# Performance work log

Hardware: AMD Instinct MI355X
Metric: run time of the kernel (lower is better)

## Reference

```python
import jax, jax.numpy as jnp
import numpy as np


def setup_inputs() -> dict:
    key = jax.random.key(0)
    k1, k2, k3, k4 = jax.random.split(key, 4)
    M, K, N = 64, 8192, 28672
    group_size = 128
    num_groups = K // group_size  # 64
    x = jax.random.normal(k1, (M, K), dtype=jnp.float16)
    # packed int4: each int32 holds one byte value in [0, 256) = two 4-bit nibbles
    weight_packed = jax.random.randint(k2, (N, K // 2), 0, 256, dtype=jnp.int32)
    # small positive per-group scales, typical of int4 quantization
    scales = (jax.random.uniform(k3, (N, num_groups), dtype=jnp.float16) * jnp.float16(0.02)
              + jnp.float16(0.001))
    bias = jax.random.normal(k4, (N,), dtype=jnp.float16) * jnp.float16(0.1)
    return {"x": x, "weight_packed": weight_packed, "scales": scales,
            "bias": bias, "group_size": group_size}


def reference(x, weight_packed, scales, bias, group_size):
    # x: [M, K] fp16; weight_packed: [N, K//2] bytes; scales: [N, K//group_size] fp16
    N, Khalf = weight_packed.shape
    K = 2 * Khalf
    num_groups = K // group_size
    # unpack nibbles: low nibble = even K index, high nibble = odd K index
    low = weight_packed & 0xF
    high = (weight_packed >> 4) & 0xF
    w_int = jnp.stack([low, high], axis=-1).reshape(N, K)  # [N, K] in [0, 16)
    # dequantize with zero-point 8 and per-group scales
    w = (w_int.astype(jnp.float16) - jnp.float16(8.0)).reshape(N, num_groups, group_size)
    w = (w * scales[:, :, None]).reshape(N, K)  # [N, K] fp16
    out = jnp.einsum("mk,nk->mn", x, w)  # [M, N] fp16
    return out + bias[None, :]
```

## Files before the change

### kernel.cpp

```cpp
#include <hip/hip_runtime.h>
#include <stdint.h>


typedef __attribute__((ext_vector_type(8))) short     short8;
typedef __attribute__((ext_vector_type(4))) float     f32x4;
typedef __attribute__((ext_vector_type(4))) int       i32x4;
typedef __attribute__((ext_vector_type(2))) _Float16  f16x2;
typedef __attribute__((ext_vector_type(8))) _Float16  f16x8;

static __device__ __forceinline__ void gload_lds16(const void* gp, void* lp) {
    __builtin_amdgcn_global_load_lds(
        (const __attribute__((address_space(1))) unsigned int*)gp,
        (__attribute__((address_space(3))) unsigned int*)lp, 16, 0, 0);
}

static __device__ __forceinline__ f16x8 dequant(const i32x4& w, f16x2 s2) {
    const f16x2 c1032 = {(_Float16)1032.0f, (_Float16)1032.0f};
    union { unsigned u[4]; f16x8 v; } r;
    #pragma unroll
    for (int j = 0; j < 4; ++j) {
        unsigned v = (unsigned)w[j];
        unsigned u = ((v & 0xFu) | 0x64006400u) | ((v << 12) & 0xF0000u);
        f16x2 h = __builtin_bit_cast(f16x2, u);
        h = (h - c1032) * s2;
        r.u[j] = __builtin_bit_cast(unsigned, h);
    }
    return r.v;
}

__global__ __launch_bounds__(256)
void xpack_kernel(const float* __restrict__ x, unsigned short* __restrict__ xf, int K) {
    int c    = blockIdx.x * 256 + threadIdx.x;
    int g    = c >> 10;
    int st   = (c >> 8) & 3;
    int mt   = (c >> 6) & 3;
    int lane = c & 63;
    int quad = lane >> 4, l15 = lane & 15;
    const float* p = x + (size_t)(l15 + mt * 16) * K + g * 128 + st * 32 + quad * 8;
    f32x4 lo = *(const f32x4*)p;
    f32x4 hi = *(const f32x4*)(p + 4);
    f16x8 r = { (_Float16)lo[0], (_Float16)lo[1], (_Float16)lo[2], (_Float16)lo[3],
                (_Float16)hi[0], (_Float16)hi[1], (_Float16)hi[2], (_Float16)hi[3] };
    *(short8*)(xf + (size_t)c * 8) = __builtin_bit_cast(short8, r);
}

__global__ __launch_bounds__(256)
void int4mm_kernel(const unsigned short* __restrict__ xf,
                   const int*   __restrict__ wp,
                   const float* __restrict__ sc,
                   const float* __restrict__ bias,
                   float*       __restrict__ out,
                   int K, int N)
{
    __shared__ char lds[49152];
    char*  ldsW = lds;
    float* ldsS = (float*)(lds + 32768);

    const int tid  = threadIdx.x;
    const int lane = tid & 63;
    const int wave = tid >> 6;
    const int quad = lane >> 4;
    const int l15  = lane & 15;
    const int blk64 = blockIdx.x * 64;
    const int ng   = K / 128;

    const char* wp8 = (const char*)wp;

    unsigned woff[4];
    #pragma unroll
    for (int j = 0; j < 4; ++j) {
        int cloc  = wave * 16 + j * 4 + quad;
        int chunk = l15 ^ (j * 4 + quad);
        woff[j] = ((unsigned)(blk64 + cloc) << 14) + ((unsigned)chunk << 4);
    }

    int rdW[4];
    #pragma unroll
    for (int nt = 0; nt < 4; ++nt)
        rdW[nt] = (nt * 16 + l15) * 256 + (((wave * 4 + quad) ^ l15) << 4);

    {
        const int c  = tid & 63;
        const int g0 = (tid >> 6) * 16;
        const float* sp = sc + (size_t)(blk64 + c) * ng + g0;
        f32x4 s0 = *(const f32x4*)(sp);
        f32x4 s1 = *(const f32x4*)(sp + 4);
        f32x4 s2 = *(const f32x4*)(sp + 8);
        f32x4 s3 = *(const f32x4*)(sp + 12);
        #pragma unroll
        for (int j = 0; j < 4; ++j) {
            ldsS[(g0 + 0  + j) * 64 + c] = s0[j];
            ldsS[(g0 + 4  + j) * 64 + c] = s1[j];
            ldsS[(g0 + 8  + j) * 64 + c] = s2[j];
            ldsS[(g0 + 12 + j) * 64 + c] = s3[j];
        }
    }
    #pragma unroll
    for (int j = 0; j < 4; ++j)
        gload_lds16(wp8 + woff[j], ldsW + (wave * 4 + j) * 1024);

    const char* xbase = (const char*)xf + wave * 4096 + lane * 16;
    f16x8 xn[4], xc[4];
    #pragma unroll
    for (int mt = 0; mt < 4; ++mt)
        xn[mt] = *(const f16x8*)(xbase + mt * 1024);

    f32x4 acc[4][4];
    #pragma unroll
    for (int mt = 0; mt < 4; ++mt)
        #pragma unroll
        for (int nt = 0; nt < 4; ++nt)
            acc[mt][nt] = f32x4{0.f, 0.f, 0.f, 0.f};

    __syncthreads();

    #pragma unroll 1
    for (int g = 0; g < ng; ++g) {
        const int p  = g & 1;
        const int gn = (g + 1 < ng) ? g + 1 : ng - 1;

        #pragma unroll
        for (int mt = 0; mt < 4; ++mt) xc[mt] = xn[mt];

        const char* xs = xbase + (size_t)gn * 16384;
        #pragma unroll
        for (int mt = 0; mt < 4; ++mt)
            xn[mt] = *(const f16x8*)(xs + mt * 1024);

        __builtin_amdgcn_s_barrier();

        #pragma unroll
        for (int j = 0; j < 4; ++j)
            gload_lds16(wp8 + woff[j] + (size_t)gn * 256,
                        ldsW + (p ^ 1) * 16384 + (wave * 4 + j) * 1024);

        asm volatile("s_waitcnt vmcnt(8)" ::: "memory");
        __builtin_amdgcn_s_barrier();
        __builtin_amdgcn_sched_barrier(0);

        const char* wb = ldsW + p * 16384;
        i32x4 v0 = *(const i32x4*)(wb + rdW[0]);
        i32x4 v1 = *(const i32x4*)(wb + rdW[1]);
        i32x4 v2 = *(const i32x4*)(wb + rdW[2]);
        i32x4 v3 = *(const i32x4*)(wb + rdW[3]);

        const float* sg = ldsS + g * 64;
        const float sf0 = sg[l15], sf1 = sg[16 + l15];
        const float sf2 = sg[32 + l15], sf3 = sg[48 + l15];

        {
            f16x8 b = dequant(v0, f16x2{(_Float16)sf0, (_Float16)sf0});
            #pragma unroll
            for (int mt = 0; mt < 4; ++mt)
                acc[mt][0] = __builtin_amdgcn_mfma_f32_16x16x32_f16(xc[mt], b, acc[mt][0], 0, 0, 0);
        }
        {
            f16x8 b = dequant(v1, f16x2{(_Float16)sf1, (_Float16)sf1});
            #pragma unroll
            for (int mt = 0; mt < 4; ++mt)
                acc[mt][1] = __builtin_amdgcn_mfma_f32_16x16x32_f16(xc[mt], b, acc[mt][1], 0, 0, 0);
        }
        {
            f16x8 b = dequant(v2, f16x2{(_Float16)sf2, (_Float16)sf2});
            #pragma unroll
            for (int mt = 0; mt < 4; ++mt)
                acc[mt][2] = __builtin_amdgcn_mfma_f32_16x16x32_f16(xc[mt], b, acc[mt][2], 0, 0, 0);
        }
        {
            f16x8 b = dequant(v3, f16x2{(_Float16)sf3, (_Float16)sf3});
            #pragma unroll
            for (int mt = 0; mt < 4; ++mt)
                acc[mt][3] = __builtin_amdgcn_mfma_f32_16x16x32_f16(xc[mt], b, acc[mt][3], 0, 0, 0);
        }
    }

    __syncthreads();
    #pragma unroll
    for (int o = 0; o < 4; ++o) {
        if (o == wave) continue;
        const int s = wave - (wave > o ? 1 : 0);
        #pragma unroll
        for (int nt = 0; nt < 4; ++nt)
            *(f32x4*)(lds + (size_t)(((o * 3 + s) * 4 + nt) * 1024) + lane * 16)
                = acc[o][nt];
    }
    __syncthreads();

    f32x4 own[4];
    #pragma unroll
    for (int nt = 0; nt < 4; ++nt) own[nt] = acc[0][nt];
    #pragma unroll
    for (int o = 1; o < 4; ++o)
        if (wave == o) {
            own[0] = acc[o][0]; own[1] = acc[o][1];
            own[2] = acc[o][2]; own[3] = acc[o][3];
        }
    #pragma unroll
    for (int s = 0; s < 3; ++s)
        #pragma unroll
        for (int nt = 0; nt < 4; ++nt)
            own[nt] += *(const f32x4*)(lds + (size_t)(((wave * 3 + s) * 4 + nt) * 1024)
                                       + lane * 16);

    #pragma unroll
    for (int nt = 0; nt < 4; ++nt) {
        const int col = blk64 + nt * 16 + l15;
        const float bv = bias[col];
        #pragma unroll
        for (int r = 0; r < 4; ++r)
            out[(size_t)(wave * 16 + quad * 4 + r) * N + col] = own[nt][r] + bv;
    }
}

extern "C" void kernel_launch(void* const* d_in, const int* in_sizes, int n_in,
                              void* d_out, int out_size, void* d_ws, size_t ws_size,
                              hipStream_t stream)
{
    const float* x    = (const float*)d_in[0];
    const int*   wp   = (const int*)d_in[1];
    const float* sc   = (const float*)d_in[2];
    const float* bias = (const float*)d_in[3];
    float*       out  = (float*)d_out;

    const int N  = in_sizes[3];
    const long long Kh = (long long)in_sizes[1] / N;
    const int K  = (int)(2 * Kh);
    const int ng = K / 128;

    unsigned short* xf = (unsigned short*)d_ws;

    xpack_kernel<<<(ng * 1024) / 256, 256, 0, stream>>>(x, xf, K);
    int4mm_kernel<<<N / 64, 256, 0, stream>>>(xf, wp, sc, bias, out, K, N);
}
```

Measured before the change: 107.2 us.

## Shrink int4 GEMM block tile from 64 to 16 output columns for more blocks

Each block now computes 16 output columns instead of 64. That gives four times as many blocks (1792 instead of 448), cuts LDS use from 48KB to 12KB, and adds a launch-bounds hint for 4 blocks per SM so occupancy rises. The goal is better latency hiding and fuller use of the 256 CUs in this memory-bound weight stream. The cost is that every block re-reads all of x, which is four times more activation traffic (served from L2), and there are fewer MFMAs per barrier per iteration.

```diff
diff --git a/kernel.cpp b/kernel.cpp
--- a/kernel.cpp
+++ b/kernel.cpp
@@ -44,7 +44,7 @@
     *(short8*)(xf + (size_t)c * 8) = __builtin_bit_cast(short8, r);
 }
 
-__global__ __launch_bounds__(256)
+__global__ __launch_bounds__(256, 4)
 void int4mm_kernel(const unsigned short* __restrict__ xf,
                    const int*   __restrict__ wp,
                    const float* __restrict__ sc,
@@ -52,52 +52,37 @@
                    float*       __restrict__ out,
                    int K, int N)
 {
-    __shared__ char lds[49152];
+    __shared__ char lds[12288];
     char*  ldsW = lds;
-    float* ldsS = (float*)(lds + 32768);
+    float* ldsS = (float*)(lds + 8192);
 
     const int tid  = threadIdx.x;
     const int lane = tid & 63;
     const int wave = tid >> 6;
     const int quad = lane >> 4;
     const int l15  = lane & 15;
-    const int blk64 = blockIdx.x * 64;
+    const int blk16 = blockIdx.x * 16;
     const int ng   = K / 128;
 
     const char* wp8 = (const char*)wp;
 
-    unsigned woff[4];
-    #pragma unroll
-    for (int j = 0; j < 4; ++j) {
-        int cloc  = wave * 16 + j * 4 + quad;
-        int chunk = l15 ^ (j * 4 + quad);
-        woff[j] = ((unsigned)(blk64 + cloc) << 14) + ((unsigned)chunk << 4);
-    }
+    const int cloc = wave * 4 + (lane >> 4);
+    const size_t wsrc = (size_t)(blk16 + cloc) * 16384
+                      + ((size_t)(unsigned)(l15 ^ cloc) << 4);
 
-    int rdW[4];
-    #pragma unroll
-    for (int nt = 0; nt < 4; ++nt)
-        rdW[nt] = (nt * 16 + l15) * 256 + (((wave * 4 + quad) ^ l15) << 4);
+    const int q   = wave * 4 + quad;
+    const int rdW = l15 * 256 + ((q ^ l15) << 4);
 
     {
-        const int c  = tid & 63;
-        const int g0 = (tid >> 6) * 16;
-        const float* sp = sc + (size_t)(blk64 + c) * ng + g0;
-        f32x4 s0 = *(const f32x4*)(sp);
-        f32x4 s1 = *(const f32x4*)(sp + 4);
-        f32x4 s2 = *(const f32x4*)(sp + 8);
-        f32x4 s3 = *(const f32x4*)(sp + 12);
+        const int c  = tid & 15;
+        const int g0 = (tid >> 4) * 4;
+        const float* sp = sc + (size_t)(blk16 + c) * ng + g0;
+        f32x4 s = *(const f32x4*)sp;
         #pragma unroll
-        for (int j = 0; j < 4; ++j) {
-            ldsS[(g0 + 0  + j) * 64 + c] = s0[j];
-            ldsS[(g0 + 4  + j) * 64 + c] = s1[j];
-            ldsS[(g0 + 8  + j) * 64 + c] = s2[j];
-            ldsS[(g0 + 12 + j) * 64 + c] = s3[j];
-        }
+        for (int j = 0; j < 4; ++j)
+            ldsS[(g0 + j) * 16 + c] = s[j];
     }
-    #pragma unroll
-    for (int j = 0; j < 4; ++j)
-        gload_lds16(wp8 + woff[j], ldsW + (wave * 4 + j) * 1024);
+    gload_lds16(wp8 + wsrc, ldsW + wave * 1024);
 
     const char* xbase = (const char*)xf + wave * 4096 + lane * 16;
     f16x8 xn[4], xc[4];
@@ -105,12 +90,10 @@
     for (int mt = 0; mt < 4; ++mt)
         xn[mt] = *(const f16x8*)(xbase + mt * 1024);
 
-    f32x4 acc[4][4];
+    f32x4 acc[4];
     #pragma unroll
     for (int mt = 0; mt < 4; ++mt)
-        #pragma unroll
-        for (int nt = 0; nt < 4; ++nt)
-            acc[mt][nt] = f32x4{0.f, 0.f, 0.f, 0.f};
+        acc[mt] = f32x4{0.f, 0.f, 0.f, 0.f};
 
     __syncthreads();
 
@@ -129,49 +112,19 @@
 
         __builtin_amdgcn_s_barrier();
 
-        #pragma unroll
-        for (int j = 0; j < 4; ++j)
-            gload_lds16(wp8 + woff[j] + (size_t)gn * 256,
-                        ldsW + (p ^ 1) * 16384 + (wave * 4 + j) * 1024);
+        gload_lds16(wp8 + wsrc + (size_t)gn * 256,
+                    ldsW + (p ^ 1) * 4096 + wave * 1024);
 
-        asm volatile("s_waitcnt vmcnt(8)" ::: "memory");
+        asm volatile("s_waitcnt vmcnt(5)" ::: "memory");
         __builtin_amdgcn_s_barrier();
         __builtin_amdgcn_sched_barrier(0);
 
-        const char* wb = ldsW + p * 16384;
-        i32x4 v0 = *(const i32x4*)(wb + rdW[0]);
-        i32x4 v1 = *(const i32x4*)(wb + rdW[1]);
-        i32x4 v2 = *(const i32x4*)(wb + rdW[2]);
-        i32x4 v3 = *(const i32x4*)(wb + rdW[3]);
-
-        const float* sg = ldsS + g * 64;
-        const float sf0 = sg[l15], sf1 = sg[16 + l15];
-        const float sf2 = sg[32 + l15], sf3 = sg[48 + l15];
-
-        {
-            f16x8 b = dequant(v0, f16x2{(_Float16)sf0, (_Float16)sf0});
-            #pragma unroll
-            for (int mt = 0; mt < 4; ++mt)
-                acc[mt][0] = __builtin_amdgcn_mfma_f32_16x16x32_f16(xc[mt], b, acc[mt][0], 0, 0, 0);
-        }
-        {
-            f16x8 b = dequant(v1, f16x2{(_Float16)sf1, (_Float16)sf1});
-            #pragma unroll
-            for (int mt = 0; mt < 4; ++mt)
-                acc[mt][1] = __builtin_amdgcn_mfma_f32_16x16x32_f16(xc[mt], b, acc[mt][1], 0, 0, 0);
-        }
-        {
-            f16x8 b = dequant(v2, f16x2{(_Float16)sf2, (_Float16)sf2});
-            #pragma unroll
-            for (int mt = 0; mt < 4; ++mt)
-                acc[mt][2] = __builtin_amdgcn_mfma_f32_16x16x32_f16(xc[mt], b, acc[mt][2], 0, 0, 0);
-        }
-        {
-            f16x8 b = dequant(v3, f16x2{(_Float16)sf3, (_Float16)sf3});
-            #pragma unroll
-            for (int mt = 0; mt < 4; ++mt)
-                acc[mt][3] = __builtin_amdgcn_mfma_f32_16x16x32_f16(xc[mt], b, acc[mt][3], 0, 0, 0);
-        }
+        i32x4 v = *(const i32x4*)(ldsW + p * 4096 + rdW);
+        const float sf = ldsS[g * 16 + l15];
+        f16x8 b = dequant(v, f16x2{(_Float16)sf, (_Float16)sf});
+        #pragma unroll
+        for (int mt = 0; mt < 4; ++mt)
+            acc[mt] = __builtin_amdgcn_mfma_f32_16x16x32_f16(xc[mt], b, acc[mt], 0, 0, 0);
     }
 
     __syncthreads();
@@ -179,37 +132,23 @@
     for (int o = 0; o < 4; ++o) {
         if (o == wave) continue;
         const int s = wave - (wave > o ? 1 : 0);
-        #pragma unroll
-        for (int nt = 0; nt < 4; ++nt)
-            *(f32x4*)(lds + (size_t)(((o * 3 + s) * 4 + nt) * 1024) + lane * 16)
-                = acc[o][nt];
+        *(f32x4*)(lds + (size_t)((o * 3 + s) * 1024) + lane * 16) = acc[o];
     }
     __syncthreads();
 
-    f32x4 own[4];
-    #pragma unroll
-    for (int nt = 0; nt < 4; ++nt) own[nt] = acc[0][nt];
+    f32x4 own = acc[0];
     #pragma unroll
     for (int o = 1; o < 4; ++o)
-        if (wave == o) {
-            own[0] = acc[o][0]; own[1] = acc[o][1];
-            own[2] = acc[o][2]; own[3] = acc[o][3];
-        }
+        if (wave == o) own = acc[o];
     #pragma unroll
     for (int s = 0; s < 3; ++s)
-        #pragma unroll
-        for (int nt = 0; nt < 4; ++nt)
-            own[nt] += *(const f32x4*)(lds + (size_t)(((wave * 3 + s) * 4 + nt) * 1024)
-                                       + lane * 16);
+        own += *(const f32x4*)(lds + (size_t)((wave * 3 + s) * 1024) + lane * 16);
 
+    const int col = blk16 + l15;
+    const float bv = bias[col];
     #pragma unroll
-    for (int nt = 0; nt < 4; ++nt) {
-        const int col = blk64 + nt * 16 + l15;
-        const float bv = bias[col];
-        #pragma unroll
-        for (int r = 0; r < 4; ++r)
-            out[(size_t)(wave * 16 + quad * 4 + r) * N + col] = own[nt][r] + bv;
-    }
+    for (int r = 0; r < 4; ++r)
+        out[(size_t)(wave * 16 + quad * 4 + r) * N + col] = own[r] + bv;
 }
 
 extern "C" void kernel_launch(void* const* d_in, const int* in_sizes, int n_in,
@@ -230,5 +169,5 @@
     unsigned short* xf = (unsigned short*)d_ws;
 
     xpack_kernel<<<(ng * 1024) / 256, 256, 0, stream>>>(x, xf, K);
-    int4mm_kernel<<<N / 64, 256, 0, stream>>>(xf, wp, sc, bias, out, K, N);
+    int4mm_kernel<<<N / 16, 256, 0, stream>>>(xf, wp, sc, bias, out, K, N);
 }
```

After: 162.3 us. 1.51x slower.

## Process two K-groups per pipeline stage with larger double-buffered weight tiles

Applied to the files above, without the earlier changes.

The main loop now covers two 128-wide K groups per iteration, staging 32KB of packed weights per buffer (64KB double-buffered). This halves the number of barrier pairs and makes each async load batch larger, so more bytes are in flight per wave. The four dequants per group are done up front before the MFMA block, and the x fragments for the next stage are loaded after use. LDS grows to 80KB and launch bounds request 2 blocks per CU, which may limit occupancy and add register pressure.

```diff
diff --git a/kernel.cpp b/kernel.cpp
--- a/kernel.cpp
+++ b/kernel.cpp
@@ -44,7 +44,7 @@
     *(short8*)(xf + (size_t)c * 8) = __builtin_bit_cast(short8, r);
 }
 
-__global__ __launch_bounds__(256)
+__global__ __launch_bounds__(256, 2)
 void int4mm_kernel(const unsigned short* __restrict__ xf,
                    const int*   __restrict__ wp,
                    const float* __restrict__ sc,
@@ -52,9 +52,9 @@
                    float*       __restrict__ out,
                    int K, int N)
 {
-    __shared__ char lds[49152];
+    __shared__ char lds[81920];
     char*  ldsW = lds;
-    float* ldsS = (float*)(lds + 32768);
+    float* ldsS = (float*)(lds + 65536);
 
     const int tid  = threadIdx.x;
     const int lane = tid & 63;
@@ -63,21 +63,26 @@
     const int l15  = lane & 15;
     const int blk64 = blockIdx.x * 64;
     const int ng   = K / 128;
+    const int ns   = ng / 2;
 
     const char* wp8 = (const char*)wp;
 
-    unsigned woff[4];
-    #pragma unroll
-    for (int j = 0; j < 4; ++j) {
-        int cloc  = wave * 16 + j * 4 + quad;
-        int chunk = l15 ^ (j * 4 + quad);
+    unsigned woff[8];
+    #pragma unroll
+    for (int j = 0; j < 8; ++j) {
+        const int cloc  = (wave * 8 + j) * 2 + (lane >> 5);
+        const int chunk = (lane & 31) ^ (cloc & 31);
         woff[j] = ((unsigned)(blk64 + cloc) << 14) + ((unsigned)chunk << 4);
     }
 
-    int rdW[4];
-    #pragma unroll
-    for (int nt = 0; nt < 4; ++nt)
-        rdW[nt] = (nt * 16 + l15) * 256 + (((wave * 4 + quad) ^ l15) << 4);
+    const int q = wave * 4 + quad;
+    int rdA[4], rdB[4];
+    #pragma unroll
+    for (int nt = 0; nt < 4; ++nt) {
+        const int base = (nt * 16 + l15) * 512 + ((q ^ l15) << 4);
+        rdA[nt] = base + (((0 ^ (nt & 1)) * 16) << 4);
+        rdB[nt] = base + (((1 ^ (nt & 1)) * 16) << 4);
+    }
 
     {
         const int c  = tid & 63;
@@ -96,14 +101,17 @@
         }
     }
     #pragma unroll
-    for (int j = 0; j < 4; ++j)
-        gload_lds16(wp8 + woff[j], ldsW + (wave * 4 + j) * 1024);
+    for (int j = 0; j < 8; ++j)
+        gload_lds16(wp8 + woff[j], ldsW + (wave * 8 + j) * 1024);
 
     const char* xbase = (const char*)xf + wave * 4096 + lane * 16;
-    f16x8 xn[4], xc[4];
+    f16x8 xa[4], xb[4];
     #pragma unroll
     for (int mt = 0; mt < 4; ++mt)
-        xn[mt] = *(const f16x8*)(xbase + mt * 1024);
+        xa[mt] = *(const f16x8*)(xbase + mt * 1024);
+    #pragma unroll
+    for (int mt = 0; mt < 4; ++mt)
+        xb[mt] = *(const f16x8*)(xbase + 16384 + mt * 1024);
 
     f32x4 acc[4][4];
     #pragma unroll
@@ -115,62 +123,73 @@
     __syncthreads();
 
     #pragma unroll 1
-    for (int g = 0; g < ng; ++g) {
-        const int p  = g & 1;
-        const int gn = (g + 1 < ng) ? g + 1 : ng - 1;
-
-        #pragma unroll
-        for (int mt = 0; mt < 4; ++mt) xc[mt] = xn[mt];
-
-        const char* xs = xbase + (size_t)gn * 16384;
-        #pragma unroll
-        for (int mt = 0; mt < 4; ++mt)
-            xn[mt] = *(const f16x8*)(xs + mt * 1024);
+    for (int s = 0; s < ns; ++s) {
+        const int p  = s & 1;
+        const int sn = (s + 1 < ns) ? s + 1 : ns - 1;
+        const int gA = 2 * s, gB = 2 * s + 1;
+        const int nA = (gA + 2 < ng) ? gA + 2 : ng - 1;
+        const int nB = (gB + 2 < ng) ? gB + 2 : ng - 1;
 
         __builtin_amdgcn_s_barrier();
 
         #pragma unroll
-        for (int j = 0; j < 4; ++j)
-            gload_lds16(wp8 + woff[j] + (size_t)gn * 256,
-                        ldsW + (p ^ 1) * 16384 + (wave * 4 + j) * 1024);
-
-        asm volatile("s_waitcnt vmcnt(8)" ::: "memory");
+        for (int j = 0; j < 8; ++j)
+            gload_lds16(wp8 + woff[j] + (size_t)sn * 512,
+                        ldsW + (p ^ 1) * 32768 + (wave * 8 + j) * 1024);
+
+        asm volatile("s_waitcnt vmcnt(16)" ::: "memory");
         __builtin_amdgcn_s_barrier();
         __builtin_amdgcn_sched_barrier(0);
 
-        const char* wb = ldsW + p * 16384;
-        i32x4 v0 = *(const i32x4*)(wb + rdW[0]);
-        i32x4 v1 = *(const i32x4*)(wb + rdW[1]);
-        i32x4 v2 = *(const i32x4*)(wb + rdW[2]);
-        i32x4 v3 = *(const i32x4*)(wb + rdW[3]);
-
-        const float* sg = ldsS + g * 64;
-        const float sf0 = sg[l15], sf1 = sg[16 + l15];
-        const float sf2 = sg[32 + l15], sf3 = sg[48 + l15];
+        const char* wb = ldsW + p * 32768;
+        const float* sgA = ldsS + gA * 64;
+        const float* sgB = ldsS + gB * 64;
 
         {
-            f16x8 b = dequant(v0, f16x2{(_Float16)sf0, (_Float16)sf0});
+            i32x4 v0 = *(const i32x4*)(wb + rdA[0]);
+            i32x4 v1 = *(const i32x4*)(wb + rdA[1]);
+            i32x4 v2 = *(const i32x4*)(wb + rdA[2]);
+            i32x4 v3 = *(const i32x4*)(wb + rdA[3]);
+            const float sf0 = sgA[l15], sf1 = sgA[16 + l15];
+            const float sf2 = sgA[32 + l15], sf3 = sgA[48 + l15];
+            f16x8 b0 = dequant(v0, f16x2{(_Float16)sf0, (_Float16)sf0});
+            f16x8 b1 = dequant(v1, f16x2{(_Float16)sf1, (_Float16)sf1});
+            f16x8 b2 = dequant(v2, f16x2{(_Float16)sf2, (_Float16)sf2});
+            f16x8 b3 = dequant(v3, f16x2{(_Float16)sf3, (_Float16)sf3});
+            #pragma unroll
+            for (int mt = 0; mt < 4; ++mt) {
+                acc[mt][0] = __builtin_amdgcn_mfma_f32_16x16x32_f16(xa[mt], b0, acc[mt][0], 0, 0, 0);
+                acc[mt][1] = __builtin_amdgcn_mfma_f32_16x16x32_f16(xa[mt], b1, acc[mt][1], 0, 0, 0);
+                acc[mt][2] = __builtin_amdgcn_mfma_f32_16x16x32_f16(xa[mt], b2, acc[mt][2], 0, 0, 0);
+                acc[mt][3] = __builtin_amdgcn_mfma_f32_16x16x32_f16(xa[mt], b3, acc[mt][3], 0, 0, 0);
+            }
+            const char* xs = xbase + (size_t)nA * 16384;
             #pragma unroll
             for (int mt = 0; mt < 4; ++mt)
-                acc[mt][0] = __builtin_amdgcn_mfma_f32_16x16x32_f16(xc[mt], b, acc[mt][0], 0, 0, 0);
+                xa[mt] = *(const f16x8*)(xs + mt * 1024);
         }
         {
-            f16x8 b = dequant(v1, f16x2{(_Float16)sf1, (_Float16)sf1});
+            i32x4 v0 = *(const i32x4*)(wb + rdB[0]);
+            i32x4 v1 = *(const i32x4*)(wb + rdB[1]);
+            i32x4 v2 = *(const i32x4*)(wb + rdB[2]);
+            i32x4 v3 = *(const i32x4*)(wb + rdB[3]);
+            const float sf0 = sgB[l15], sf1 = sgB[16 + l15];
+            const float sf2 = sgB[32 + l15], sf3 = sgB[48 + l15];
+            f16x8 b0 = dequant(v0, f16x2{(_Float16)sf0, (_Float16)sf0});
+            f16x8 b1 = dequant(v1, f16x2{(_Float16)sf1, (_Float16)sf1});
+            f16x8 b2 = dequant(v2, f16x2{(_Float16)sf2, (_Float16)sf2});
+            f16x8 b3 = dequant(v3, f16x2{(_Float16)sf3, (_Float16)sf3});
+            #pragma unroll
+            for (int mt = 0; mt < 4; ++mt) {
+                acc[mt][0] = __builtin_amdgcn_mfma_f32_16x16x32_f16(xb[mt], b0, acc[mt][0], 0, 0, 0);
+                acc[mt][1] = __builtin_amdgcn_mfma_f32_16x16x32_f16(xb[mt], b1, acc[mt][1], 0, 0, 0);
+                acc[mt][2] = __builtin_amdgcn_mfma_f32_16x16x32_f16(xb[mt], b2, acc[mt][2], 0, 0, 0);
+                acc[mt][3] = __builtin_amdgcn_mfma_f32_16x16x32_f16(xb[mt], b3, acc[mt][3], 0, 0, 0);
+            }
+            const char* xs = xbase + (size_t)nB * 16384;
             #pragma unroll
             for (int mt = 0; mt < 4; ++mt)
-                acc[mt][1] = __builtin_amdgcn_mfma_f32_16x16x32_f16(xc[mt], b, acc[mt][1], 0, 0, 0);
-        }
-        {
-            f16x8 b = dequant(v2, f16x2{(_Float16)sf2, (_Float16)sf2});
-            #pragma unroll
-            for (int mt = 0; mt < 4; ++mt)
-                acc[mt][2] = __builtin_amdgcn_mfma_f32_16x16x32_f16(xc[mt], b, acc[mt][2], 0, 0, 0);
-        }
-        {
-            f16x8 b = dequant(v3, f16x2{(_Float16)sf3, (_Float16)sf3});
-            #pragma unroll
-            for (int mt = 0; mt < 4; ++mt)
-                acc[mt][3] = __builtin_amdgcn_mfma_f32_16x16x32_f16(xc[mt], b, acc[mt][3], 0, 0, 0);
+                xb[mt] = *(const f16x8*)(xs + mt * 1024);
         }
     }
 
```

New measurement: 104.5 us. 1.03x faster.

## Split int4 GEMM into producer/consumer waves with LDS ring and atomic flags

Applied to the files above, without the earlier changes.

The main kernel now runs 8 waves: 4 producer waves stream packed weights into a 4-slot LDS ring with global_load_lds, and 4 consumer waves dequantize and issue MFMAs. Block-wide barriers are replaced by workgroup-scope atomic counters. Scales are pre-transposed by a new kernel so consumers can load them directly from global memory with prefetch. This aims to hide weight-load latency behind compute, at the cost of spin-wait overhead, an extra kernel launch, and more LDS per block, which may reduce occupancy.

```diff
diff --git a/kernel.cpp b/kernel.cpp
--- a/kernel.cpp
+++ b/kernel.cpp
@@ -7,6 +7,8 @@
 typedef __attribute__((ext_vector_type(4))) int       i32x4;
 typedef __attribute__((ext_vector_type(2))) _Float16  f16x2;
 typedef __attribute__((ext_vector_type(8))) _Float16  f16x8;
+
+#define RING 4
 
 static __device__ __forceinline__ void gload_lds16(const void* gp, void* lp) {
     __builtin_amdgcn_global_load_lds(
@@ -26,6 +28,11 @@
         r.u[j] = __builtin_bit_cast(unsigned, h);
     }
     return r.v;
+}
+
+static __device__ __forceinline__ void signal1(int* f, int lane) {
+    if (lane == 0)
+        __hip_atomic_fetch_add(f, 1, __ATOMIC_RELEASE, __HIP_MEMORY_SCOPE_WORKGROUP);
 }
 
 __global__ __launch_bounds__(256)
@@ -45,65 +52,33 @@
 }
 
 __global__ __launch_bounds__(256)
+void strans_kernel(const float* __restrict__ sc, float* __restrict__ sct, int N, int ng) {
+    int n = blockIdx.x * 256 + threadIdx.x;
+    int g = blockIdx.y;
+    sct[(size_t)g * N + n] = sc[(size_t)n * ng + g];
+}
+
+__global__ __launch_bounds__(512, 4)
 void int4mm_kernel(const unsigned short* __restrict__ xf,
                    const int*   __restrict__ wp,
-                   const float* __restrict__ sc,
+                   const float* __restrict__ sct,
                    const float* __restrict__ bias,
                    float*       __restrict__ out,
                    int K, int N)
 {
-    __shared__ char lds[49152];
-    char*  ldsW = lds;
-    float* ldsS = (float*)(lds + 32768);
+    __shared__ char ldsW[RING * 16384];
+    __shared__ int  prodDone[64];
+    __shared__ int  consDone[64];
 
     const int tid  = threadIdx.x;
+    const int wave = tid >> 6;
     const int lane = tid & 63;
-    const int wave = tid >> 6;
     const int quad = lane >> 4;
     const int l15  = lane & 15;
     const int blk64 = blockIdx.x * 64;
     const int ng   = K / 128;
 
-    const char* wp8 = (const char*)wp;
-
-    unsigned woff[4];
-    #pragma unroll
-    for (int j = 0; j < 4; ++j) {
-        int cloc  = wave * 16 + j * 4 + quad;
-        int chunk = l15 ^ (j * 4 + quad);
-        woff[j] = ((unsigned)(blk64 + cloc) << 14) + ((unsigned)chunk << 4);
-    }
-
-    int rdW[4];
-    #pragma unroll
-    for (int nt = 0; nt < 4; ++nt)
-        rdW[nt] = (nt * 16 + l15) * 256 + (((wave * 4 + quad) ^ l15) << 4);
-
-    {
-        const int c  = tid & 63;
-        const int g0 = (tid >> 6) * 16;
-        const float* sp = sc + (size_t)(blk64 + c) * ng + g0;
-        f32x4 s0 = *(const f32x4*)(sp);
-        f32x4 s1 = *(const f32x4*)(sp + 4);
-        f32x4 s2 = *(const f32x4*)(sp + 8);
-        f32x4 s3 = *(const f32x4*)(sp + 12);
-        #pragma unroll
-        for (int j = 0; j < 4; ++j) {
-            ldsS[(g0 + 0  + j) * 64 + c] = s0[j];
-            ldsS[(g0 + 4  + j) * 64 + c] = s1[j];
-            ldsS[(g0 + 8  + j) * 64 + c] = s2[j];
-            ldsS[(g0 + 12 + j) * 64 + c] = s3[j];
-        }
-    }
-    #pragma unroll
-    for (int j = 0; j < 4; ++j)
-        gload_lds16(wp8 + woff[j], ldsW + (wave * 4 + j) * 1024);
-
-    const char* xbase = (const char*)xf + wave * 4096 + lane * 16;
-    f16x8 xn[4], xc[4];
-    #pragma unroll
-    for (int mt = 0; mt < 4; ++mt)
-        xn[mt] = *(const f16x8*)(xbase + mt * 1024);
+    if (tid < 64) { prodDone[tid] = 0; consDone[tid] = 0; }
 
     f32x4 acc[4][4];
     #pragma unroll
@@ -114,101 +89,150 @@
 
     __syncthreads();
 
-    #pragma unroll 1
-    for (int g = 0; g < ng; ++g) {
-        const int p  = g & 1;
-        const int gn = (g + 1 < ng) ? g + 1 : ng - 1;
-
-        #pragma unroll
-        for (int mt = 0; mt < 4; ++mt) xc[mt] = xn[mt];
-
-        const char* xs = xbase + (size_t)gn * 16384;
+    if (wave < 4) {
+        const int p = wave;
+        const char* wp8 = (const char*)wp;
+        unsigned woff[4];
+        #pragma unroll
+        for (int j = 0; j < 4; ++j) {
+            const int cloc  = p * 16 + j * 4 + quad;
+            const int chunk = l15 ^ (j * 4 + quad);
+            woff[j] = ((unsigned)(blk64 + cloc) << 14) + ((unsigned)chunk << 4);
+        }
+        #pragma unroll 1
+        for (int g = 0; g < ng; ++g) {
+            if (g >= RING) {
+                while (__hip_atomic_load(&consDone[g - RING], __ATOMIC_ACQUIRE,
+                                         __HIP_MEMORY_SCOPE_WORKGROUP) < 4)
+                    __builtin_amdgcn_s_sleep(1);
+            }
+            char* slot = ldsW + (size_t)(g & (RING - 1)) * 16384;
+            #pragma unroll
+            for (int j = 0; j < 4; ++j)
+                gload_lds16(wp8 + woff[j] + (size_t)g * 256,
+                            slot + (p * 4 + j) * 1024);
+            asm volatile("s_waitcnt vmcnt(8)" ::: "memory");
+            if (g >= 2) signal1(&prodDone[g - 2], lane);
+        }
+        asm volatile("s_waitcnt vmcnt(4)" ::: "memory");
+        signal1(&prodDone[ng - 2], lane);
+        asm volatile("s_waitcnt vmcnt(0)" ::: "memory");
+        signal1(&prodDone[ng - 1], lane);
+    } else {
+        const int kst = wave - 4;
+        const int q   = kst * 4 + quad;
+        int rdW[4];
+        #pragma unroll
+        for (int nt = 0; nt < 4; ++nt)
+            rdW[nt] = (nt * 16 + l15) * 256 + ((q ^ l15) << 4);
+
+        const char* xbase = (const char*)xf + kst * 4096 + lane * 16;
+        f16x8 xn[4];
         #pragma unroll
         for (int mt = 0; mt < 4; ++mt)
-            xn[mt] = *(const f16x8*)(xs + mt * 1024);
-
-        __builtin_amdgcn_s_barrier();
-
-        #pragma unroll
-        for (int j = 0; j < 4; ++j)
-            gload_lds16(wp8 + woff[j] + (size_t)gn * 256,
-                        ldsW + (p ^ 1) * 16384 + (wave * 4 + j) * 1024);
-
-        asm volatile("s_waitcnt vmcnt(8)" ::: "memory");
-        __builtin_amdgcn_s_barrier();
-        __builtin_amdgcn_sched_barrier(0);
-
-        const char* wb = ldsW + p * 16384;
-        i32x4 v0 = *(const i32x4*)(wb + rdW[0]);
-        i32x4 v1 = *(const i32x4*)(wb + rdW[1]);
-        i32x4 v2 = *(const i32x4*)(wb + rdW[2]);
-        i32x4 v3 = *(const i32x4*)(wb + rdW[3]);
-
-        const float* sg = ldsS + g * 64;
-        const float sf0 = sg[l15], sf1 = sg[16 + l15];
-        const float sf2 = sg[32 + l15], sf3 = sg[48 + l15];
-
-        {
-            f16x8 b = dequant(v0, f16x2{(_Float16)sf0, (_Float16)sf0});
+            xn[mt] = *(const f16x8*)(xbase + mt * 1024);
+
+        float sfn[4], sfu[4];
+        #pragma unroll
+        for (int nt = 0; nt < 4; ++nt)
+            sfn[nt] = sct[blk64 + nt * 16 + l15];
+
+        #pragma unroll 1
+        for (int g = 0; g < ng; ++g) {
+            const int gn = (g + 1 < ng) ? g + 1 : ng - 1;
+
+            while (__hip_atomic_load(&prodDone[g], __ATOMIC_ACQUIRE,
+                                     __HIP_MEMORY_SCOPE_WORKGROUP) < 4)
+                __builtin_amdgcn_s_sleep(1);
+            __builtin_amdgcn_sched_barrier(0);
+
+            const char* wb = ldsW + (size_t)(g & (RING - 1)) * 16384;
+            i32x4 v0 = *(const i32x4*)(wb + rdW[0]);
+            i32x4 v1 = *(const i32x4*)(wb + rdW[1]);
+            i32x4 v2 = *(const i32x4*)(wb + rdW[2]);
+            i32x4 v3 = *(const i32x4*)(wb + rdW[3]);
+
+            #pragma unroll
+            for (int nt = 0; nt < 4; ++nt) sfu[nt] = sfn[nt];
+            const float* sp = sct + (size_t)gn * N + blk64;
+            #pragma unroll
+            for (int nt = 0; nt < 4; ++nt)
+                sfn[nt] = sp[nt * 16 + l15];
+
+            {
+                f16x8 b = dequant(v0, f16x2{(_Float16)sfu[0], (_Float16)sfu[0]});
+                #pragma unroll
+                for (int mt = 0; mt < 4; ++mt)
+                    acc[mt][0] = __builtin_amdgcn_mfma_f32_16x16x32_f16(xn[mt], b, acc[mt][0], 0, 0, 0);
+            }
+            {
+                f16x8 b = dequant(v1, f16x2{(_Float16)sfu[1], (_Float16)sfu[1]});
+                #pragma unroll
+                for (int mt = 0; mt < 4; ++mt)
+                    acc[mt][1] = __builtin_amdgcn_mfma_f32_16x16x32_f16(xn[mt], b, acc[mt][1], 0, 0, 0);
+            }
+            {
+                f16x8 b = dequant(v2, f16x2{(_Float16)sfu[2], (_Float16)sfu[2]});
+                #pragma unroll
+                for (int mt = 0; mt < 4; ++mt)
+                    acc[mt][2] = __builtin_amdgcn_mfma_f32_16x16x32_f16(xn[mt], b, acc[mt][2], 0, 0, 0);
+            }
+            {
+                f16x8 b = dequant(v3, f16x2{(_Float16)sfu[3], (_Float16)sfu[3]});
+                #pragma unroll
+                for (int mt = 0; mt < 4; ++mt)
+                    acc[mt][3] = __builtin_amdgcn_mfma_f32_16x16x32_f16(xn[mt], b, acc[mt][3], 0, 0, 0);
+            }
+
+            asm volatile("s_waitcnt lgkmcnt(0)" ::: "memory");
+            signal1(&consDone[g], lane);
+
+            const char* xs = xbase + (size_t)gn * 16384;
             #pragma unroll
             for (int mt = 0; mt < 4; ++mt)
-                acc[mt][0] = __builtin_amdgcn_mfma_f32_16x16x32_f16(xc[mt], b, acc[mt][0], 0, 0, 0);
-        }
-        {
-            f16x8 b = dequant(v1, f16x2{(_Float16)sf1, (_Float16)sf1});
-            #pragma unroll
-            for (int mt = 0; mt < 4; ++mt)
-                acc[mt][1] = __builtin_amdgcn_mfma_f32_16x16x32_f16(xc[mt], b, acc[mt][1], 0, 0, 0);
-        }
-        {
-            f16x8 b = dequant(v2, f16x2{(_Float16)sf2, (_Float16)sf2});
-            #pragma unroll
-            for (int mt = 0; mt < 4; ++mt)
-                acc[mt][2] = __builtin_amdgcn_mfma_f32_16x16x32_f16(xc[mt], b, acc[mt][2], 0, 0, 0);
-        }
-        {
-            f16x8 b = dequant(v3, f16x2{(_Float16)sf3, (_Float16)sf3});
-            #pragma unroll
-            for (int mt = 0; mt < 4; ++mt)
-                acc[mt][3] = __builtin_amdgcn_mfma_f32_16x16x32_f16(xc[mt], b, acc[mt][3], 0, 0, 0);
+                xn[mt] = *(const f16x8*)(xs + mt * 1024);
         }
     }
 
     __syncthreads();
-    #pragma unroll
-    for (int o = 0; o < 4; ++o) {
-        if (o == wave) continue;
-        const int s = wave - (wave > o ? 1 : 0);
-        #pragma unroll
-        for (int nt = 0; nt < 4; ++nt)
-            *(f32x4*)(lds + (size_t)(((o * 3 + s) * 4 + nt) * 1024) + lane * 16)
-                = acc[o][nt];
+    if (wave >= 4) {
+        const int kst = wave - 4;
+        #pragma unroll
+        for (int o = 0; o < 4; ++o) {
+            if (o == kst) continue;
+            const int s = kst - (kst > o ? 1 : 0);
+            #pragma unroll
+            for (int nt = 0; nt < 4; ++nt)
+                *(f32x4*)(ldsW + (size_t)(((o * 3 + s) * 4 + nt) * 1024) + lane * 16)
+                    = acc[o][nt];
+        }
     }
     __syncthreads();
-
-    f32x4 own[4];
-    #pragma unroll
-    for (int nt = 0; nt < 4; ++nt) own[nt] = acc[0][nt];
-    #pragma unroll
-    for (int o = 1; o < 4; ++o)
-        if (wave == o) {
-            own[0] = acc[o][0]; own[1] = acc[o][1];
-            own[2] = acc[o][2]; own[3] = acc[o][3];
-        }
-    #pragma unroll
-    for (int s = 0; s < 3; ++s)
-        #pragma unroll
-        for (int nt = 0; nt < 4; ++nt)
-            own[nt] += *(const f32x4*)(lds + (size_t)(((wave * 3 + s) * 4 + nt) * 1024)
-                                       + lane * 16);
-
-    #pragma unroll
-    for (int nt = 0; nt < 4; ++nt) {
-        const int col = blk64 + nt * 16 + l15;
-        const float bv = bias[col];
-        #pragma unroll
-        for (int r = 0; r < 4; ++r)
-            out[(size_t)(wave * 16 + quad * 4 + r) * N + col] = own[nt][r] + bv;
+    if (wave >= 4) {
+        const int kst = wave - 4;
+        f32x4 own[4];
+        #pragma unroll
+        for (int nt = 0; nt < 4; ++nt) own[nt] = acc[0][nt];
+        #pragma unroll
+        for (int o = 1; o < 4; ++o)
+            if (kst == o) {
+                own[0] = acc[o][0]; own[1] = acc[o][1];
+                own[2] = acc[o][2]; own[3] = acc[o][3];
+            }
+        #pragma unroll
+        for (int s = 0; s < 3; ++s)
+            #pragma unroll
+            for (int nt = 0; nt < 4; ++nt)
+                own[nt] += *(const f32x4*)(ldsW + (size_t)(((kst * 3 + s) * 4 + nt) * 1024)
+                                           + lane * 16);
+        #pragma unroll
+        for (int nt = 0; nt < 4; ++nt) {
+            const int col = blk64 + nt * 16 + l15;
+            const float bv = bias[col];
+            #pragma unroll
+            for (int r = 0; r < 4; ++r)
+                out[(size_t)(kst * 16 + quad * 4 + r) * N + col] = own[nt][r] + bv;
+        }
     }
 }
 
@@ -228,7 +252,10 @@
     const int ng = K / 128;
 
     unsigned short* xf = (unsigned short*)d_ws;
+    const size_t xf_bytes = (size_t)ng * 16384;
+    float* sct = (float*)((char*)d_ws + xf_bytes);
 
     xpack_kernel<<<(ng * 1024) / 256, 256, 0, stream>>>(x, xf, K);
-    int4mm_kernel<<<N / 64, 256, 0, stream>>>(xf, wp, sc, bias, out, K, N);
-}
+    strans_kernel<<<dim3(N / 256, ng), 256, 0, stream>>>(sc, sct, N, ng);
+    int4mm_kernel<<<N / 64, 512, 0, stream>>>(xf, wp, sct, bias, out, K, N);
+}
```

After: 131.6 us. 22.8% more time.
